# Performance work log

Measured on AMD Instinct MI355X. Metric: run time of the kernel, lower is better.

## Reference

```python
import jax, jax.numpy as jnp
import numpy as np

T, KBLK, EMB, B = 2048, 64, 512, 4


def _make_coords(t, k):
    # head1: for each j, cols = block_start(j) + arange(j % k + 1)  (block-causal local)
    j = np.arange(t)
    cnt1 = (j % k) + 1
    rows1 = np.repeat(j, cnt1)
    off1 = np.arange(cnt1.sum()) - np.repeat(np.cumsum(cnt1) - cnt1, cnt1)
    cols1 = (rows1 // k) * k + off1
    # head2: for each block start c, rows = arange(c, t), col = c  (strided block-start)
    starts = np.arange(t // k) * k
    cnt2 = t - starts
    base = np.repeat(starts, cnt2)
    off2 = np.arange(cnt2.sum()) - np.repeat(np.cumsum(cnt2) - cnt2, cnt2)
    rows2, cols2 = base + off2, base
    c1 = np.stack([rows1, cols1], 1).astype(np.int32)
    c2 = np.stack([rows2, cols2], 1).astype(np.int32)
    return c1, c2


def setup_inputs() -> dict:
    key = jax.random.key(0)
    ks = jax.random.split(key, 6)
    s = 1.0 / float(np.sqrt(EMB))
    c1, c2 = _make_coords(T, KBLK)
    return {
        "x": jax.random.normal(ks[0], (B, T, EMB), jnp.float32),
        "Wk": jax.random.normal(ks[1], (EMB, EMB), jnp.float32) * s,
        "bk": jnp.zeros((EMB,), jnp.float32),
        "Wq": jax.random.normal(ks[2], (EMB, EMB), jnp.float32) * s,
        "bq": jnp.zeros((EMB,), jnp.float32),
        "Wv": jax.random.normal(ks[3], (EMB, EMB), jnp.float32) * s,
        "bv": jnp.zeros((EMB,), jnp.float32),
        "Wu": jax.random.normal(ks[4], (EMB, 2 * EMB), jnp.float32) * s,
        "bu": jnp.zeros((EMB,), jnp.float32),
        "coords1": jnp.asarray(c1),
        "coords2": jnp.asarray(c2),
    }


def _sparse_head(Kt, Qt, Vt, coords):
    rows, cols = coords[:, 0], coords[:, 1]
    # dot[b,p] = (K @ Q^T)[b, rows[p], cols[p]] = K[b,rows[p],:] . Q[b,cols[p],:]
    dot = jnp.einsum('bpe,bpe->bp', Kt[:, rows], Qt[:, cols])
    # sparse.batchmm: out[b,r] = sum_{p: rows[p]=r} dot[b,p] * V[b, cols[p]]
    out = jnp.zeros_like(Vt).at[:, rows].add(dot[..., None] * Vt[:, cols])
    return out


def reference(x, Wk, bk, Wq, bq, Wv, bv, Wu, bu, coords1, coords2):
    Kt = x @ Wk.T + bk
    Qt = x @ Wq.T + bq
    Vt = x @ Wv.T + bv
    h1 = _sparse_head(Kt, Qt, Vt, coords1)
    h2 = _sparse_head(Kt, Qt, Vt, coords2)
    comb = jnp.concatenate([h1, h2], axis=-1)  # [B, T, 2*EMB]
    return comb @ Wu.T + bu
```

## Files before the change

kernel.cpp:

```cpp
#include <hip/hip_runtime.h>


typedef unsigned short u16;
typedef __attribute__((ext_vector_type(8))) short short8;
typedef __attribute__((ext_vector_type(4))) float f32x4;

constexpr int TDIM  = 2048;
constexpr int EMB_D = 512;
constexpr int BB    = 4;
constexpr int NBLK  = 32;

__device__ __forceinline__ u16 f2b(float f) {
    unsigned u = __float_as_uint(f);
    unsigned r = (u + 0x7FFFu + ((u >> 16) & 1u)) >> 16;
    return (u16)r;
}

template<bool U16OUT, int BN>
__device__ __forceinline__ void gemm_core(
    const u16* __restrict__ A, int lda,
    const u16* __restrict__ W, int ldw,
    const float* __restrict__ bias,
    void* __restrict__ Cp, int ldc, int K,
    int bm, int bn)
{
    __shared__ u16 As[128 * 32];
    __shared__ u16 Bs[BN * 32];
    constexpr int NT = BN / 32;
    const int tid  = threadIdx.x;
    const int wid  = tid >> 6;
    const int lane = tid & 63;
    const int l15  = lane & 15;
    const int quad = lane >> 4;
    const int wm = (wid & 1) * 64;
    const int wn = (wid >> 1) * (BN / 2);

    f32x4 acc[4][NT] = {};

    const int srow  = tid >> 2;
    const int skoff = (tid & 3) * 8;
    const u16* Ag = A + (size_t)(bm + srow) * lda + skoff;
    const u16* Wg = W + (size_t)(bn + srow) * ldw + skoff;
    char* AsBase = (char*)As + wid * 1024;
    char* BsBase = (char*)Bs + wid * 1024;

    for (int k0 = 0; k0 < K; k0 += 32) {
        __syncthreads();
        __builtin_amdgcn_global_load_lds(
            (const __attribute__((address_space(1))) void*)(Ag + k0),
            (__attribute__((address_space(3))) void*)AsBase, 16, 0, 0);
        __builtin_amdgcn_global_load_lds(
            (const __attribute__((address_space(1))) void*)(Ag + (size_t)64 * lda + k0),
            (__attribute__((address_space(3))) void*)(AsBase + 4096), 16, 0, 0);
        __builtin_amdgcn_global_load_lds(
            (const __attribute__((address_space(1))) void*)(Wg + k0),
            (__attribute__((address_space(3))) void*)BsBase, 16, 0, 0);
        if (BN == 128)
            __builtin_amdgcn_global_load_lds(
                (const __attribute__((address_space(1))) void*)(Wg + (size_t)64 * ldw + k0),
                (__attribute__((address_space(3))) void*)(BsBase + 4096), 16, 0, 0);
        __syncthreads();

        short8 a[4], b[NT];
        #pragma unroll
        for (int i = 0; i < 4; ++i)
            a[i] = *(const short8*)((const short*)As + (wm + 16 * i + l15) * 32 + quad * 8);
        #pragma unroll
        for (int j = 0; j < NT; ++j)
            b[j] = *(const short8*)((const short*)Bs + (wn + 16 * j + l15) * 32 + quad * 8);
        #pragma unroll
        for (int i = 0; i < 4; ++i)
            #pragma unroll
            for (int j = 0; j < NT; ++j)
                acc[i][j] = __builtin_amdgcn_mfma_f32_16x16x32_bf16(a[i], b[j], acc[i][j], 0, 0, 0);
    }

    #pragma unroll
    for (int i = 0; i < 4; ++i) {
        #pragma unroll
        for (int j = 0; j < NT; ++j) {
            const int col = bn + wn + 16 * j + l15;
            const float bv = bias[col];
            #pragma unroll
            for (int r = 0; r < 4; ++r) {
                const int row = bm + wm + 16 * i + quad * 4 + r;
                if (U16OUT) ((u16*)Cp)[(size_t)row * ldc + col] = f2b(acc[i][j][r] + bv);
                else        ((float*)Cp)[(size_t)row * ldc + col] = acc[i][j][r] + bv;
            }
        }
    }
}

__global__ __launch_bounds__(256) void qkv_gemm_k(
    const u16* __restrict__ xb,
    const u16* __restrict__ wkb, const u16* __restrict__ wqb, const u16* __restrict__ wvb,
    const float* __restrict__ bk, const float* __restrict__ bq, const float* __restrict__ bv,
    u16* __restrict__ Ktb, u16* __restrict__ Qtb, u16* __restrict__ Vtb)
{
    const u16* W; const float* bias; u16* C;
    if (blockIdx.z == 0)      { W = wkb; bias = bk; C = Ktb; }
    else if (blockIdx.z == 1) { W = wqb; bias = bq; C = Qtb; }
    else                      { W = wvb; bias = bv; C = Vtb; }
    gemm_core<true, 64>(xb, EMB_D, W, EMB_D, bias, C, EMB_D, EMB_D,
                        blockIdx.x * 128, blockIdx.y * 64);
}

__global__ __launch_bounds__(256) void out_gemm_k(
    const u16* __restrict__ combb, const u16* __restrict__ wub,
    const float* __restrict__ bu, float* __restrict__ out)
{
    gemm_core<false, 64>(combb, 2 * EMB_D, wub, 2 * EMB_D, bu, out, EMB_D, 2 * EMB_D,
                         blockIdx.x * 128, blockIdx.y * 64);
}

__global__ __launch_bounds__(256) void cast_k(
    const float* __restrict__ x, const float* __restrict__ wk, const float* __restrict__ wq,
    const float* __restrict__ wv, const float* __restrict__ wu,
    u16* __restrict__ xb, u16* __restrict__ wkb, u16* __restrict__ wqb,
    u16* __restrict__ wvb, u16* __restrict__ wub)
{
    const int s = blockIdx.y;
    int n; const float* src; u16* dst;
    switch (s) {
        case 0: n = 4194304; src = x;  dst = xb;  break;
        case 1: n = 262144;  src = wk; dst = wkb; break;
        case 2: n = 262144;  src = wq; dst = wqb; break;
        case 3: n = 262144;  src = wv; dst = wvb; break;
        default: n = 524288; src = wu; dst = wub; break;
    }
    const int idx = (blockIdx.x * 256 + threadIdx.x) * 4;
    if (idx >= n) return;
    float4 v = *(const float4*)(src + idx);
    ushort4 o = { f2b(v.x), f2b(v.y), f2b(v.z), f2b(v.w) };
    *(ushort4*)(dst + idx) = o;
}

__global__ __launch_bounds__(256) void heads_k(
    const u16* __restrict__ Ktb, const u16* __restrict__ Qtb,
    const u16* __restrict__ Vtb, u16* __restrict__ comb)
{
    __shared__ u16 sm1[64 * 72];
    __shared__ u16 sm2[128 * 72];
    const int blk = blockIdx.x, b = blockIdx.y, z = blockIdx.z;
    const int tid = threadIdx.x;
    const int wid = tid >> 6, lane = tid & 63;
    const int l15 = lane & 15, quad = lane >> 4;
    const size_t row0 = (size_t)b * TDIM + (size_t)blk * 64;
    const int srow_base = 16 * wid + quad * 4;

    if (z < 4) {
        const int e0 = z * 128;
        f32x4 s[4] = {};
        const u16* Kp = Ktb + (row0 + 16 * wid + l15) * EMB_D + quad * 8;
        const u16* Qp = Qtb + (row0 + l15) * EMB_D + quad * 8;
        for (int ks = 0; ks < 16; ++ks) {
            short8 af = *(const short8*)(Kp + 32 * ks);
            #pragma unroll
            for (int j = 0; j < 4; ++j) {
                short8 bf = *(const short8*)(Qp + (size_t)(16 * j) * EMB_D + 32 * ks);
                s[j] = __builtin_amdgcn_mfma_f32_16x16x32_bf16(af, bf, s[j], 0, 0, 0);
            }
        }
        #pragma unroll
        for (int j = 0; j < 4; ++j)
            #pragma unroll
            for (int r = 0; r < 4; ++r) {
                const int rr = srow_base + r;
                const int cc = 16 * j + l15;
                sm1[rr * 72 + cc] = f2b((cc <= rr) ? s[j][r] : 0.0f);
            }
        #pragma unroll
        for (int it = 0; it < 4; ++it) {
            const int id = tid + 256 * it;
            const int c  = id & 63;
            const int eo = (id >> 6) * 8;
            short8 v = *(const short8*)(Vtb + (row0 + c) * EMB_D + e0 + eo);
            #pragma unroll
            for (int i = 0; i < 8; ++i) sm2[(eo + i) * 72 + c] = (u16)v[i];
        }
        __syncthreads();
        f32x4 o[8] = {};
        const u16* arow = sm1 + (16 * wid + l15) * 72;
        #pragma unroll
        for (int ks = 0; ks < 2; ++ks) {
            short8 as = *(const short8*)(arow + 32 * ks + quad * 8);
            #pragma unroll
            for (int nt = 0; nt < 8; ++nt) {
                short8 bs = *(const short8*)(sm2 + (16 * nt + l15) * 72 + 32 * ks + quad * 8);
                o[nt] = __builtin_amdgcn_mfma_f32_16x16x32_bf16(as, bs, o[nt], 0, 0, 0);
            }
        }
        #pragma unroll
        for (int nt = 0; nt < 8; ++nt)
            #pragma unroll
            for (int r = 0; r < 4; ++r)
                comb[(row0 + srow_base + r) * (2 * EMB_D) + e0 + 16 * nt + l15] = f2b(o[nt][r]);
    } else {
        const int R = blk;
        const int e0 = (z - 4) * 128;
        f32x4 s[2] = {};
        const u16* Kp = Ktb + (row0 + 16 * wid + l15) * EMB_D + quad * 8;
        const u16* Qp = Qtb + ((size_t)b * TDIM + (size_t)64 * l15) * EMB_D + quad * 8;
        for (int ks = 0; ks < 16; ++ks) {
            short8 af = *(const short8*)(Kp + 32 * ks);
            #pragma unroll
            for (int j = 0; j < 2; ++j) {
                short8 bf = *(const short8*)(Qp + (size_t)(64 * 16 * j) * EMB_D + 32 * ks);
                s[j] = __builtin_amdgcn_mfma_f32_16x16x32_bf16(af, bf, s[j], 0, 0, 0);
            }
        }
        #pragma unroll
        for (int j = 0; j < 2; ++j)
            #pragma unroll
            for (int r = 0; r < 4; ++r) {
                const int m  = 16 * j + l15;
                const int rr = srow_base + r;
                sm1[rr * 40 + m] = f2b((m <= R) ? s[j][r] : 0.0f);
            }
        #pragma unroll
        for (int it = 0; it < 2; ++it) {
            const int id = tid + 256 * it;
            const int m  = id & 31;
            const int eo = (id >> 5) * 8;
            short8 v = *(const short8*)(Vtb + ((size_t)b * TDIM + 64 * m) * EMB_D + e0 + eo);
            #pragma unroll
            for (int i = 0; i < 8; ++i) sm2[(eo + i) * 40 + m] = (u16)v[i];
        }
        __syncthreads();
        f32x4 o[8] = {};
        short8 as = *(const short8*)(sm1 + (16 * wid + l15) * 40 + quad * 8);
        #pragma unroll
        for (int nt = 0; nt < 8; ++nt) {
            short8 bs = *(const short8*)(sm2 + (16 * nt + l15) * 40 + quad * 8);
            o[nt] = __builtin_amdgcn_mfma_f32_16x16x32_bf16(as, bs, o[nt], 0, 0, 0);
        }
        #pragma unroll
        for (int nt = 0; nt < 8; ++nt)
            #pragma unroll
            for (int r = 0; r < 4; ++r)
                comb[(row0 + srow_base + r) * (2 * EMB_D) + EMB_D + e0 + 16 * nt + l15] = f2b(o[nt][r]);
    }
}

extern "C" void kernel_launch(void* const* d_in, const int* in_sizes, int n_in,
                              void* d_out, int out_size, void* d_ws, size_t ws_size,
                              hipStream_t stream)
{
    const float* x  = (const float*)d_in[0];
    const float* Wk = (const float*)d_in[1];
    const float* bk = (const float*)d_in[2];
    const float* Wq = (const float*)d_in[3];
    const float* bq = (const float*)d_in[4];
    const float* Wv = (const float*)d_in[5];
    const float* bv = (const float*)d_in[6];
    const float* Wu = (const float*)d_in[7];
    const float* bu = (const float*)d_in[8];
    float* out = (float*)d_out;

    char* w = (char*)d_ws;
    u16* Ktb   = (u16*)(w + ((size_t)0  << 20));
    u16* Qtb   = (u16*)(w + ((size_t)8  << 20));
    u16* Vtb   = (u16*)(w + ((size_t)16 << 20));
    u16* combb = (u16*)(w + ((size_t)24 << 20));
    u16* xb    = (u16*)(w + ((size_t)40 << 20));
    u16* wkb   = (u16*)(w + ((size_t)48 << 20));
    u16* wqb   = (u16*)(w + ((size_t)49 << 20));
    u16* wvb   = (u16*)(w + ((size_t)50 << 20));
    u16* wub   = (u16*)(w + ((size_t)51 << 20));

    dim3 blk(256);
    hipLaunchKernelGGL(cast_k, dim3(4096, 5), blk, 0, stream,
                       x, Wk, Wq, Wv, Wu, xb, wkb, wqb, wvb, wub);
    hipLaunchKernelGGL(qkv_gemm_k, dim3(64, 8, 3), blk, 0, stream,
                       xb, wkb, wqb, wvb, bk, bq, bv, Ktb, Qtb, Vtb);
    hipLaunchKernelGGL(heads_k, dim3(NBLK, BB, 8), blk, 0, stream,
                       Ktb, Qtb, Vtb, combb);
    hipLaunchKernelGGL(out_gemm_k, dim3(64, 8), blk, 0, stream,
                       combb, wub, bu, out);
}
```

Baseline: 165.2 us.

## Fold output projection into V weights and fuse heads with output GEMM

Precomputes Wu_half·Wv products (and matching biases) so the projected value vectors for each head come straight out of one concatenated K/Q/V' GEMM with 2048 output columns. The heads kernel then merges both sparse heads into a single 96-wide contraction and writes final fp32 output plus bias directly, removing the comb intermediate and the separate output GEMM. This costs an extra small fp32 weight-product kernel per call and a wider projection GEMM, and changes bf16 rounding points.

```diff
diff --git a/kernel.cpp b/kernel.cpp
--- a/kernel.cpp
+++ b/kernel.cpp
@@ -9,6 +9,7 @@
 constexpr int EMB_D = 512;
 constexpr int BB    = 4;
 constexpr int NBLK  = 32;
+constexpr int LDK   = 2048;
 
 __device__ __forceinline__ u16 f2b(float f) {
     unsigned u = __float_as_uint(f);
@@ -16,229 +17,237 @@
     return (u16)r;
 }
 
-template<bool U16OUT, int BN>
-__device__ __forceinline__ void gemm_core(
-    const u16* __restrict__ A, int lda,
-    const u16* __restrict__ W, int ldw,
-    const float* __restrict__ bias,
-    void* __restrict__ Cp, int ldc, int K,
-    int bm, int bn)
+__global__ __launch_bounds__(256) void cast_k(
+    const float* __restrict__ x, const float* __restrict__ wk, const float* __restrict__ wq,
+    u16* __restrict__ xb, u16* __restrict__ wcat)
+{
+    const int s = blockIdx.y;
+    int n; const float* src; u16* dst;
+    if (s == 0)      { n = 4194304; src = x;  dst = xb; }
+    else if (s == 1) { n = 262144;  src = wk; dst = wcat; }
+    else             { n = 262144;  src = wq; dst = wcat + 262144; }
+    const int idx = (blockIdx.x * 256 + threadIdx.x) * 4;
+    if (idx >= n) return;
+    float4 v = *(const float4*)(src + idx);
+    ushort4 o = { f2b(v.x), f2b(v.y), f2b(v.z), f2b(v.w) };
+    *(ushort4*)(dst + idx) = o;
+}
+
+__global__ __launch_bounds__(256) void wc_k(
+    const float* __restrict__ Wu, const float* __restrict__ Wv, u16* __restrict__ wcat)
+{
+    const int half = blockIdx.z;
+    const int bn = blockIdx.x * 64, bkc = blockIdx.y * 64;
+    __shared__ float As[16][64];
+    __shared__ float Bs[16][64];
+    const int tid = threadIdx.x, tx = tid & 15, ty = tid >> 4;
+    const int lm = tid >> 2, lj = (tid & 3) << 2;
+    float acc[4][4] = {};
+    for (int j0 = 0; j0 < 512; j0 += 16) {
+        float4 av = *(const float4*)(Wu + (size_t)(bn + lm) * 1024 + half * 512 + j0 + lj);
+        float4 bw = *(const float4*)(Wv + (size_t)(j0 + ty) * 512 + bkc + tx * 4);
+        __syncthreads();
+        As[lj+0][lm]=av.x; As[lj+1][lm]=av.y; As[lj+2][lm]=av.z; As[lj+3][lm]=av.w;
+        *(float4*)(&Bs[ty][tx*4]) = bw;
+        __syncthreads();
+        #pragma unroll
+        for (int kk = 0; kk < 16; ++kk) {
+            float ar[4], br[4];
+            #pragma unroll
+            for (int i=0;i<4;i++) ar[i]=As[kk][(ty<<2)+i];
+            float4 bb = *(const float4*)(&Bs[kk][tx<<2]);
+            br[0]=bb.x; br[1]=bb.y; br[2]=bb.z; br[3]=bb.w;
+            #pragma unroll
+            for (int i=0;i<4;i++)
+                #pragma unroll
+                for (int l=0;l<4;l++)
+                    acc[i][l] += ar[i]*br[l];
+        }
+    }
+    #pragma unroll
+    for (int i=0;i<4;i++) {
+        const int n = bn + (ty<<2) + i;
+        #pragma unroll
+        for (int l=0;l<4;l++)
+            wcat[(size_t)(1024 + half*512 + n) * 512 + bkc + (tx<<2) + l] = f2b(acc[i][l]);
+    }
+}
+
+__global__ __launch_bounds__(256) void bias_k(
+    const float* __restrict__ bk, const float* __restrict__ bq,
+    const float* __restrict__ bv, const float* __restrict__ Wu,
+    float* __restrict__ biascat)
+{
+    const int g = blockIdx.x * 256 + threadIdx.x;
+    if (g < 512) biascat[g] = bk[g];
+    else if (g < 1024) biascat[g] = bq[g - 512];
+    else {
+        const int n = (g - 1024) & 511;
+        const int half = (g - 1024) >> 9;
+        float s = 0.f;
+        const float* wr = Wu + (size_t)n * 1024 + half * 512;
+        for (int j = 0; j < 512; j += 4) {
+            float4 a = *(const float4*)(wr + j);
+            float4 b = *(const float4*)(bv + j);
+            s += a.x*b.x + a.y*b.y + a.z*b.z + a.w*b.w;
+        }
+        biascat[g] = s;
+    }
+}
+
+__global__ __launch_bounds__(256) void kqv_gemm_k(
+    const u16* __restrict__ A, const u16* __restrict__ W,
+    const float* __restrict__ bias, u16* __restrict__ C)
 {
     __shared__ u16 As[128 * 32];
-    __shared__ u16 Bs[BN * 32];
-    constexpr int NT = BN / 32;
+    __shared__ u16 Bs[128 * 32];
+    const int bm = blockIdx.x * 128;
+    const int bn = blockIdx.y * 128;
     const int tid  = threadIdx.x;
     const int wid  = tid >> 6;
     const int lane = tid & 63;
     const int l15  = lane & 15;
     const int quad = lane >> 4;
     const int wm = (wid & 1) * 64;
-    const int wn = (wid >> 1) * (BN / 2);
-
-    f32x4 acc[4][NT] = {};
+    const int wn = (wid >> 1) * 64;
+
+    f32x4 acc[4][4] = {};
 
     const int srow  = tid >> 2;
     const int skoff = (tid & 3) * 8;
-    const u16* Ag = A + (size_t)(bm + srow) * lda + skoff;
-    const u16* Wg = W + (size_t)(bn + srow) * ldw + skoff;
+    const u16* Ag = A + (size_t)(bm + srow) * EMB_D + skoff;
+    const u16* Wg = W + (size_t)(bn + srow) * EMB_D + skoff;
     char* AsBase = (char*)As + wid * 1024;
     char* BsBase = (char*)Bs + wid * 1024;
 
-    for (int k0 = 0; k0 < K; k0 += 32) {
+    for (int k0 = 0; k0 < EMB_D; k0 += 32) {
         __syncthreads();
         __builtin_amdgcn_global_load_lds(
             (const __attribute__((address_space(1))) void*)(Ag + k0),
             (__attribute__((address_space(3))) void*)AsBase, 16, 0, 0);
         __builtin_amdgcn_global_load_lds(
-            (const __attribute__((address_space(1))) void*)(Ag + (size_t)64 * lda + k0),
+            (const __attribute__((address_space(1))) void*)(Ag + (size_t)64 * EMB_D + k0),
             (__attribute__((address_space(3))) void*)(AsBase + 4096), 16, 0, 0);
         __builtin_amdgcn_global_load_lds(
             (const __attribute__((address_space(1))) void*)(Wg + k0),
             (__attribute__((address_space(3))) void*)BsBase, 16, 0, 0);
-        if (BN == 128)
-            __builtin_amdgcn_global_load_lds(
-                (const __attribute__((address_space(1))) void*)(Wg + (size_t)64 * ldw + k0),
-                (__attribute__((address_space(3))) void*)(BsBase + 4096), 16, 0, 0);
-        __syncthreads();
-
-        short8 a[4], b[NT];
+        __builtin_amdgcn_global_load_lds(
+            (const __attribute__((address_space(1))) void*)(Wg + (size_t)64 * EMB_D + k0),
+            (__attribute__((address_space(3))) void*)(BsBase + 4096), 16, 0, 0);
+        __syncthreads();
+
+        short8 a[4], b[4];
         #pragma unroll
         for (int i = 0; i < 4; ++i)
             a[i] = *(const short8*)((const short*)As + (wm + 16 * i + l15) * 32 + quad * 8);
         #pragma unroll
-        for (int j = 0; j < NT; ++j)
+        for (int j = 0; j < 4; ++j)
             b[j] = *(const short8*)((const short*)Bs + (wn + 16 * j + l15) * 32 + quad * 8);
         #pragma unroll
         for (int i = 0; i < 4; ++i)
             #pragma unroll
-            for (int j = 0; j < NT; ++j)
+            for (int j = 0; j < 4; ++j)
                 acc[i][j] = __builtin_amdgcn_mfma_f32_16x16x32_bf16(a[i], b[j], acc[i][j], 0, 0, 0);
     }
 
     #pragma unroll
     for (int i = 0; i < 4; ++i) {
         #pragma unroll
-        for (int j = 0; j < NT; ++j) {
+        for (int j = 0; j < 4; ++j) {
             const int col = bn + wn + 16 * j + l15;
-            const float bv = bias[col];
+            const float bvv = bias[col];
             #pragma unroll
             for (int r = 0; r < 4; ++r) {
                 const int row = bm + wm + 16 * i + quad * 4 + r;
-                if (U16OUT) ((u16*)Cp)[(size_t)row * ldc + col] = f2b(acc[i][j][r] + bv);
-                else        ((float*)Cp)[(size_t)row * ldc + col] = acc[i][j][r] + bv;
+                C[(size_t)row * LDK + col] = f2b(acc[i][j][r] + bvv);
             }
         }
     }
 }
 
-__global__ __launch_bounds__(256) void qkv_gemm_k(
-    const u16* __restrict__ xb,
-    const u16* __restrict__ wkb, const u16* __restrict__ wqb, const u16* __restrict__ wvb,
-    const float* __restrict__ bk, const float* __restrict__ bq, const float* __restrict__ bv,
-    u16* __restrict__ Ktb, u16* __restrict__ Qtb, u16* __restrict__ Vtb)
-{
-    const u16* W; const float* bias; u16* C;
-    if (blockIdx.z == 0)      { W = wkb; bias = bk; C = Ktb; }
-    else if (blockIdx.z == 1) { W = wqb; bias = bq; C = Qtb; }
-    else                      { W = wvb; bias = bv; C = Vtb; }
-    gemm_core<true, 64>(xb, EMB_D, W, EMB_D, bias, C, EMB_D, EMB_D,
-                        blockIdx.x * 128, blockIdx.y * 64);
-}
-
-__global__ __launch_bounds__(256) void out_gemm_k(
-    const u16* __restrict__ combb, const u16* __restrict__ wub,
-    const float* __restrict__ bu, float* __restrict__ out)
-{
-    gemm_core<false, 64>(combb, 2 * EMB_D, wub, 2 * EMB_D, bu, out, EMB_D, 2 * EMB_D,
-                         blockIdx.x * 128, blockIdx.y * 64);
-}
-
-__global__ __launch_bounds__(256) void cast_k(
-    const float* __restrict__ x, const float* __restrict__ wk, const float* __restrict__ wq,
-    const float* __restrict__ wv, const float* __restrict__ wu,
-    u16* __restrict__ xb, u16* __restrict__ wkb, u16* __restrict__ wqb,
-    u16* __restrict__ wvb, u16* __restrict__ wub)
-{
-    const int s = blockIdx.y;
-    int n; const float* src; u16* dst;
-    switch (s) {
-        case 0: n = 4194304; src = x;  dst = xb;  break;
-        case 1: n = 262144;  src = wk; dst = wkb; break;
-        case 2: n = 262144;  src = wq; dst = wqb; break;
-        case 3: n = 262144;  src = wv; dst = wvb; break;
-        default: n = 524288; src = wu; dst = wub; break;
-    }
-    const int idx = (blockIdx.x * 256 + threadIdx.x) * 4;
-    if (idx >= n) return;
-    float4 v = *(const float4*)(src + idx);
-    ushort4 o = { f2b(v.x), f2b(v.y), f2b(v.z), f2b(v.w) };
-    *(ushort4*)(dst + idx) = o;
-}
-
 __global__ __launch_bounds__(256) void heads_k(
-    const u16* __restrict__ Ktb, const u16* __restrict__ Qtb,
-    const u16* __restrict__ Vtb, u16* __restrict__ comb)
-{
-    __shared__ u16 sm1[64 * 72];
-    __shared__ u16 sm2[128 * 72];
-    const int blk = blockIdx.x, b = blockIdx.y, z = blockIdx.z;
+    const u16* __restrict__ KQV, const float* __restrict__ bu, float* __restrict__ out)
+{
+    __shared__ u16 sm1[64 * 104];
+    __shared__ u16 sm2[128 * 104];
+    const int blk = blockIdx.x, b = blockIdx.y;
+    const int e0 = blockIdx.z * 128;
     const int tid = threadIdx.x;
     const int wid = tid >> 6, lane = tid & 63;
     const int l15 = lane & 15, quad = lane >> 4;
     const size_t row0 = (size_t)b * TDIM + (size_t)blk * 64;
     const int srow_base = 16 * wid + quad * 4;
 
-    if (z < 4) {
-        const int e0 = z * 128;
-        f32x4 s[4] = {};
-        const u16* Kp = Ktb + (row0 + 16 * wid + l15) * EMB_D + quad * 8;
-        const u16* Qp = Qtb + (row0 + l15) * EMB_D + quad * 8;
-        for (int ks = 0; ks < 16; ++ks) {
-            short8 af = *(const short8*)(Kp + 32 * ks);
-            #pragma unroll
-            for (int j = 0; j < 4; ++j) {
-                short8 bf = *(const short8*)(Qp + (size_t)(16 * j) * EMB_D + 32 * ks);
-                s[j] = __builtin_amdgcn_mfma_f32_16x16x32_bf16(af, bf, s[j], 0, 0, 0);
-            }
-        }
-        #pragma unroll
-        for (int j = 0; j < 4; ++j)
-            #pragma unroll
-            for (int r = 0; r < 4; ++r) {
-                const int rr = srow_base + r;
-                const int cc = 16 * j + l15;
-                sm1[rr * 72 + cc] = f2b((cc <= rr) ? s[j][r] : 0.0f);
-            }
-        #pragma unroll
-        for (int it = 0; it < 4; ++it) {
-            const int id = tid + 256 * it;
-            const int c  = id & 63;
-            const int eo = (id >> 6) * 8;
-            short8 v = *(const short8*)(Vtb + (row0 + c) * EMB_D + e0 + eo);
-            #pragma unroll
-            for (int i = 0; i < 8; ++i) sm2[(eo + i) * 72 + c] = (u16)v[i];
-        }
-        __syncthreads();
-        f32x4 o[8] = {};
-        const u16* arow = sm1 + (16 * wid + l15) * 72;
-        #pragma unroll
-        for (int ks = 0; ks < 2; ++ks) {
-            short8 as = *(const short8*)(arow + 32 * ks + quad * 8);
-            #pragma unroll
-            for (int nt = 0; nt < 8; ++nt) {
-                short8 bs = *(const short8*)(sm2 + (16 * nt + l15) * 72 + 32 * ks + quad * 8);
-                o[nt] = __builtin_amdgcn_mfma_f32_16x16x32_bf16(as, bs, o[nt], 0, 0, 0);
-            }
-        }
-        #pragma unroll
-        for (int nt = 0; nt < 8; ++nt)
-            #pragma unroll
-            for (int r = 0; r < 4; ++r)
-                comb[(row0 + srow_base + r) * (2 * EMB_D) + e0 + 16 * nt + l15] = f2b(o[nt][r]);
-    } else {
-        const int R = blk;
-        const int e0 = (z - 4) * 128;
-        f32x4 s[2] = {};
-        const u16* Kp = Ktb + (row0 + 16 * wid + l15) * EMB_D + quad * 8;
-        const u16* Qp = Qtb + ((size_t)b * TDIM + (size_t)64 * l15) * EMB_D + quad * 8;
-        for (int ks = 0; ks < 16; ++ks) {
-            short8 af = *(const short8*)(Kp + 32 * ks);
-            #pragma unroll
-            for (int j = 0; j < 2; ++j) {
-                short8 bf = *(const short8*)(Qp + (size_t)(64 * 16 * j) * EMB_D + 32 * ks);
-                s[j] = __builtin_amdgcn_mfma_f32_16x16x32_bf16(af, bf, s[j], 0, 0, 0);
-            }
-        }
-        #pragma unroll
-        for (int j = 0; j < 2; ++j)
-            #pragma unroll
-            for (int r = 0; r < 4; ++r) {
-                const int m  = 16 * j + l15;
-                const int rr = srow_base + r;
-                sm1[rr * 40 + m] = f2b((m <= R) ? s[j][r] : 0.0f);
-            }
-        #pragma unroll
-        for (int it = 0; it < 2; ++it) {
-            const int id = tid + 256 * it;
-            const int m  = id & 31;
-            const int eo = (id >> 5) * 8;
-            short8 v = *(const short8*)(Vtb + ((size_t)b * TDIM + 64 * m) * EMB_D + e0 + eo);
-            #pragma unroll
-            for (int i = 0; i < 8; ++i) sm2[(eo + i) * 40 + m] = (u16)v[i];
-        }
-        __syncthreads();
-        f32x4 o[8] = {};
-        short8 as = *(const short8*)(sm1 + (16 * wid + l15) * 40 + quad * 8);
+    f32x4 s1[4] = {}; f32x4 s2[2] = {};
+    const u16* Kp  = KQV + (row0 + 16 * wid + l15) * (size_t)LDK + quad * 8;
+    const u16* Qp  = KQV + (row0 + l15) * (size_t)LDK + 512 + quad * 8;
+    const u16* Qsp = KQV + ((size_t)b * TDIM + (size_t)64 * l15) * (size_t)LDK + 512 + quad * 8;
+    for (int ks = 0; ks < 16; ++ks) {
+        short8 af = *(const short8*)(Kp + 32 * ks);
+        #pragma unroll
+        for (int j = 0; j < 4; ++j) {
+            short8 bf = *(const short8*)(Qp + (size_t)(16 * j) * LDK + 32 * ks);
+            s1[j] = __builtin_amdgcn_mfma_f32_16x16x32_bf16(af, bf, s1[j], 0, 0, 0);
+        }
+        #pragma unroll
+        for (int j = 0; j < 2; ++j) {
+            short8 bf = *(const short8*)(Qsp + (size_t)(64 * 16 * j) * LDK + 32 * ks);
+            s2[j] = __builtin_amdgcn_mfma_f32_16x16x32_bf16(af, bf, s2[j], 0, 0, 0);
+        }
+    }
+    #pragma unroll
+    for (int j = 0; j < 4; ++j)
+        #pragma unroll
+        for (int r = 0; r < 4; ++r) {
+            const int rr = srow_base + r;
+            const int cc = 16 * j + l15;
+            sm1[rr * 104 + cc] = f2b((cc <= rr) ? s1[j][r] : 0.0f);
+        }
+    #pragma unroll
+    for (int j = 0; j < 2; ++j)
+        #pragma unroll
+        for (int r = 0; r < 4; ++r) {
+            const int m  = 16 * j + l15;
+            const int rr = srow_base + r;
+            sm1[rr * 104 + 64 + m] = f2b((m <= blk) ? s2[j][r] : 0.0f);
+        }
+    #pragma unroll
+    for (int it = 0; it < 4; ++it) {
+        const int id = tid + 256 * it;
+        const int c  = id & 63;
+        const int eo = (id >> 6) * 8;
+        short8 v = *(const short8*)(KQV + (row0 + c) * (size_t)LDK + 1024 + e0 + eo);
+        #pragma unroll
+        for (int i = 0; i < 8; ++i) sm2[(eo + i) * 104 + c] = (u16)v[i];
+    }
+    #pragma unroll
+    for (int it = 0; it < 2; ++it) {
+        const int id = tid + 256 * it;
+        const int m  = id & 31;
+        const int eo = (id >> 5) * 8;
+        short8 v = *(const short8*)(KQV + ((size_t)b * TDIM + 64 * m) * (size_t)LDK + 1536 + e0 + eo);
+        #pragma unroll
+        for (int i = 0; i < 8; ++i) sm2[(eo + i) * 104 + 64 + m] = (u16)v[i];
+    }
+    __syncthreads();
+    f32x4 o[8] = {};
+    const u16* arow = sm1 + (16 * wid + l15) * 104;
+    #pragma unroll
+    for (int ks = 0; ks < 3; ++ks) {
+        short8 as = *(const short8*)(arow + 32 * ks + quad * 8);
         #pragma unroll
         for (int nt = 0; nt < 8; ++nt) {
-            short8 bs = *(const short8*)(sm2 + (16 * nt + l15) * 40 + quad * 8);
+            short8 bs = *(const short8*)(sm2 + (16 * nt + l15) * 104 + 32 * ks + quad * 8);
             o[nt] = __builtin_amdgcn_mfma_f32_16x16x32_bf16(as, bs, o[nt], 0, 0, 0);
         }
-        #pragma unroll
-        for (int nt = 0; nt < 8; ++nt)
-            #pragma unroll
-            for (int r = 0; r < 4; ++r)
-                comb[(row0 + srow_base + r) * (2 * EMB_D) + EMB_D + e0 + 16 * nt + l15] = f2b(o[nt][r]);
+    }
+    #pragma unroll
+    for (int nt = 0; nt < 8; ++nt) {
+        const int col = e0 + 16 * nt + l15;
+        const float bvv = bu[col];
+        #pragma unroll
+        for (int r = 0; r < 4; ++r)
+            out[(row0 + srow_base + r) * (size_t)EMB_D + col] = o[nt][r] + bvv;
     }
 }
 
@@ -258,23 +267,15 @@
     float* out = (float*)d_out;
 
     char* w = (char*)d_ws;
-    u16* Ktb   = (u16*)(w + ((size_t)0  << 20));
-    u16* Qtb   = (u16*)(w + ((size_t)8  << 20));
-    u16* Vtb   = (u16*)(w + ((size_t)16 << 20));
-    u16* combb = (u16*)(w + ((size_t)24 << 20));
-    u16* xb    = (u16*)(w + ((size_t)40 << 20));
-    u16* wkb   = (u16*)(w + ((size_t)48 << 20));
-    u16* wqb   = (u16*)(w + ((size_t)49 << 20));
-    u16* wvb   = (u16*)(w + ((size_t)50 << 20));
-    u16* wub   = (u16*)(w + ((size_t)51 << 20));
+    u16*   KQV     = (u16*)  (w + ((size_t)0  << 20));
+    u16*   xb      = (u16*)  (w + ((size_t)32 << 20));
+    u16*   wcat    = (u16*)  (w + ((size_t)40 << 20));
+    float* biascat = (float*)(w + ((size_t)44 << 20));
 
     dim3 blk(256);
-    hipLaunchKernelGGL(cast_k, dim3(4096, 5), blk, 0, stream,
-                       x, Wk, Wq, Wv, Wu, xb, wkb, wqb, wvb, wub);
-    hipLaunchKernelGGL(qkv_gemm_k, dim3(64, 8, 3), blk, 0, stream,
-                       xb, wkb, wqb, wvb, bk, bq, bv, Ktb, Qtb, Vtb);
-    hipLaunchKernelGGL(heads_k, dim3(NBLK, BB, 8), blk, 0, stream,
-                       Ktb, Qtb, Vtb, combb);
-    hipLaunchKernelGGL(out_gemm_k, dim3(64, 8), blk, 0, stream,
-                       combb, wub, bu, out);
-}
+    hipLaunchKernelGGL(cast_k, dim3(4096, 3), blk, 0, stream, x, Wk, Wq, xb, wcat);
+    hipLaunchKernelGGL(wc_k, dim3(8, 8, 2), blk, 0, stream, Wu, Wv, wcat);
+    hipLaunchKernelGGL(bias_k, dim3(8), blk, 0, stream, bk, bq, bv, Wu, biascat);
+    hipLaunchKernelGGL(kqv_gemm_k, dim3(64, 16), blk, 0, stream, xb, wcat, biascat, KQV);
+    hipLaunchKernelGGL(heads_k, dim3(NBLK, BB, 4), blk, 0, stream, KQV, bu, out);
+}
```

New measurement: 197.6 us. 1.2x slower.
